# Optimization experiments

Hardware: AMD Instinct MI355X
Metric: run time of the kernel (lower is better)

Reference implementation:

```python
import jax, jax.numpy as jnp
import numpy as np

MODES = 32
WIDTH = 64
FACTOR = 2
N_LAYERS = 4


def dct_matrix(N):
    # Ortho DCT-II matrix D: dct(x) along last axis = x @ D.T ; idct(y) = y @ D
    n = jnp.arange(N, dtype=jnp.float32)
    k = n[:, None]
    D = jnp.cos(jnp.pi * (n[None, :] + 0.5) * k / N) * jnp.sqrt(2.0 / N)
    D = D.at[0].mul(1.0 / jnp.sqrt(2.0))
    return D


def setup_inputs() -> dict:
    key = jax.random.key(0)
    ks = jax.random.split(key, 16)
    B, M, N, IN_DIM = 4, 256, 256, 12
    hid = WIDTH * FACTOR
    xav_f = jnp.sqrt(2.0 / (WIDTH + WIDTH))  # xavier_normal for (in,out,modes)
    inp = {
        'x': jax.random.normal(ks[0], (B, M, N, IN_DIM), jnp.float32),
        'W_in': jax.random.normal(ks[1], (WIDTH, IN_DIM), jnp.float32) * (1.0 / jnp.sqrt(IN_DIM)),
        'b_in': jnp.zeros((WIDTH,), jnp.float32),
        'fw0': jax.random.normal(ks[2], (N_LAYERS, WIDTH, WIDTH, MODES), jnp.float32) * xav_f,
        'fw1': jax.random.normal(ks[3], (N_LAYERS, WIDTH, WIDTH, MODES), jnp.float32) * xav_f,
        'ffW1': jax.random.normal(ks[4], (N_LAYERS, hid, WIDTH), jnp.float32) * (1.0 / jnp.sqrt(WIDTH)),
        'ffb1': jnp.zeros((N_LAYERS, hid), jnp.float32),
        'ffW2': jax.random.normal(ks[5], (N_LAYERS, WIDTH, hid), jnp.float32) * (1.0 / jnp.sqrt(hid)),
        'ffb2': jnp.zeros((N_LAYERS, WIDTH), jnp.float32),
        'W_o1': jax.random.normal(ks[6], (128, WIDTH), jnp.float32) * (1.0 / jnp.sqrt(WIDTH)),
        'b_o1': jnp.zeros((128,), jnp.float32),
        'W_o2': jax.random.normal(ks[7], (1, 128), jnp.float32) * (1.0 / jnp.sqrt(128.0)),
        'b_o2': jnp.zeros((1,), jnp.float32),
    }
    return inp


def forward_fourier(x, w0, w1, DM, DN):
    # x: [B, M, N, I] channels-last -> [B, I, M, N]
    x = jnp.transpose(x, (0, 3, 1, 2))
    # --- y direction: DCT along N, truncated mode mix, IDCT ---
    x_fty = jnp.einsum('bimn,kn->bimk', x, DN)            # dct, [B,I,M,N]
    xy_m = jnp.einsum('bixy,ioy->boxy', x_fty[..., :MODES], w0)  # [B,O,M,modes]
    xy = jnp.einsum('boxy,yn->boxn', xy_m, DN[:MODES, :])        # idct of zero-padded spectrum
    # --- x direction: DCT along M ---
    x2 = jnp.swapaxes(x, -1, -2)                          # [B,I,N,M]
    x_ftx = jnp.einsum('binm,km->bink', x2, DM)
    xx_m = jnp.einsum('bixy,ioy->boxy', x_ftx[..., :MODES], w1)  # [B,O,N,modes]
    xx = jnp.einsum('boxy,ym->boxm', xx_m, DM[:MODES, :])        # [B,O,N,M]
    xx = jnp.swapaxes(xx, -1, -2)                         # [B,O,M,N]
    out = xx + xy
    return jnp.transpose(out, (0, 2, 3, 1))               # [B,M,N,O]


def feed_forward(h, W1, b1, W2, b2):
    h = jax.nn.relu(h @ W1.T + b1)
    return h @ W2.T + b2


def reference(x, W_in, b_in, fw0, fw1, ffW1, ffb1, ffW2, ffb2, W_o1, b_o1, W_o2, b_o2):
    B, M, N, _ = x.shape
    DM = dct_matrix(M)
    DN = dct_matrix(N)
    x = x @ W_in.T + b_in                                  # in_proj, [B,M,N,width]
    b = x
    for i in range(N_LAYERS):
        h = forward_fourier(x, fw0[i], fw1[i], DM, DN)
        b = feed_forward(h, ffW1[i], ffb1[i], ffW2[i], ffb2[i])
        x = x + b
    # use_fork=False: out applied to the LAST backcast b
    o = jax.nn.relu(b @ W_o1.T + b_o1) * 0 + (b @ W_o1.T + b_o1)  # WNLinear has no activation
    o = b @ W_o1.T + b_o1
    forecast = o @ W_o2.T + b_o2                           # [B,M,N,1]
    return forecast
```

## Files before the change

### kernel.cpp

```cpp
#include <hip/hip_runtime.h>
#include <hip/hip_bf16.h>
#include <math.h>

#define BATCH 4
#define MMDIM 256
#define NNDIM 256
#define CH 64
#define NMODES 32
#define HID 128
#define NLAYERS 4
#define XPLANE 16777216L

typedef __attribute__((ext_vector_type(8))) short bfrag;
typedef __attribute__((ext_vector_type(8))) ushort u16x8;
typedef __attribute__((ext_vector_type(4))) float f32x4;

__device__ inline ushort f2bf(float x) {
    union { float f; uint u; } v; v.f = x;
    uint r = v.u + 0x7fff + ((v.u >> 16) & 1);
    return (ushort)(r >> 16);
}
__device__ inline float bf2f(ushort h) {
    union { uint u; float f; } v; v.u = (uint)h << 16; return v.f;
}
__device__ inline void split(float v, ushort& hi, ushort& lo) {
    __hip_bfloat16 h = __float2bfloat16(v);
    hi = __builtin_bit_cast(ushort, h);
    lo = __builtin_bit_cast(ushort, __float2bfloat16(v - __bfloat162float(h)));
}
__device__ inline ushort f2bf_hw(float v) {
    return __builtin_bit_cast(ushort, __float2bfloat16(v));
}
#define MFMA __builtin_amdgcn_mfma_f32_16x16x32_bf16


__global__ __launch_bounds__(256) void k_Tfrag(ushort* __restrict__ Tf) {
    int idx = blockIdx.x * 256 + threadIdx.x;
    int j = idx & 7, lane = (idx >> 3) & 63, ks = (idx >> 9) & 7, yt = idx >> 12;
    int k = yt * 16 + (lane & 15);
    int n = ks * 32 + ((lane >> 4) << 3) + j;
    double v = cos(M_PI * (n + 0.5) * (double)k / 256.0) * 0.08838834764831845;
    if (k == 0) v *= 0.7071067811865476;
    float vf = (float)v;
    ushort hh = f2bf(vf);
    Tf[idx] = hh; Tf[idx + 8192] = f2bf(vf - bf2f(hh));
}

__global__ __launch_bounds__(256) void k_Ttfrag(ushort* __restrict__ Ttf) {
    int idx = blockIdx.x * 256 + threadIdx.x;
    int j = idx & 7, lane = (idx >> 3) & 63, at = idx >> 9;
    int k = ((lane >> 4) << 3) + j;
    int n = at * 16 + (lane & 15);
    double v = cos(M_PI * (n + 0.5) * (double)k / 256.0) * 0.08838834764831845;
    if (k == 0) v *= 0.7071067811865476;
    float vf = (float)v;
    ushort hh = f2bf(vf);
    Ttf[idx] = hh; Ttf[idx + 8192] = f2bf(vf - bf2f(hh));
}

__global__ __launch_bounds__(256) void k_wt(const float* __restrict__ fw0, const float* __restrict__ fw1,
                                            float* __restrict__ wt01) {
    int idx = blockIdx.x * 256 + threadIdx.x;
    const float* fw = (idx < 524288) ? fw0 : fw1;
    int i2 = idx & 524287;
    int l = i2 >> 17, r = i2 & 131071;
    int y = r >> 12, i = (r >> 6) & 63, o = r & 63;
    wt01[idx] = fw[((l * 64 + i) * 64 + o) * 32 + y];
}

__global__ __launch_bounds__(256) void k_wfrag(const float* __restrict__ W,
                                               ushort* __restrict__ hi, ushort* __restrict__ lo,
                                               int N, int K) {
    int idx = blockIdx.x * 256 + threadIdx.x;
    int per_l = N * K;
    int l = idx / per_l, r = idx % per_l;
    int jj = r & 7, lane = (r >> 3) & 63;
    int ks = (r >> 9) % (K >> 5);
    int nt = r / (512 * (K >> 5));
    int row = nt * 16 + (lane & 15);
    int col = ks * 32 + ((lane >> 4) << 3) + jj;
    float v = W[(long)l * per_l + row * K + col];
    ushort h = f2bf(v);
    hi[idx] = h;
    lo[idx] = f2bf(v - bf2f(h));
}

__global__ void k_head(const float* __restrict__ W_o1, const float* __restrict__ b_o1,
                       const float* __restrict__ W_o2, const float* __restrict__ b_o2,
                       float* __restrict__ Weff, float* __restrict__ beff) {
    int c = threadIdx.x;
    float acc = 0.f;
    for (int j = 0; j < 128; j++) acc += W_o2[j] * W_o1[j * 64 + c];
    Weff[c] = acc;
    if (c == 0) {
        float bb = 0.f;
        for (int j = 0; j < 128; j++) bb += W_o2[j] * b_o1[j];
        beff[0] = bb + b_o2[0];
    }
}

__global__ __launch_bounds__(256) void k_inproj_bf(const float* __restrict__ xin,
                                                   const float* __restrict__ W_in,
                                                   const float* __restrict__ b_in,
                                                   ushort* __restrict__ xbf) {
    __shared__ __align__(16) ushort tile[2][64][72];
    int t = threadIdx.x;
    int bid = blockIdx.x;
    int b = bid >> 10, m = (bid >> 2) & 255, n0 = (bid & 3) * 64;
    int c = t & 63, ng = t >> 6;
    long pbase = (long)(b * 256 + m) * 256 + n0;
    float w[12];
#pragma unroll
    for (int d = 0; d < 12; d++) w[d] = W_in[c * 12 + d];
    float bc = b_in[c];
#pragma unroll 4
    for (int i = 0; i < 16; i++) {
        int nl = ng * 16 + i;
        const float* xr = xin + (pbase + nl) * 12;
        float acc = bc;
#pragma unroll
        for (int d = 0; d < 12; d++) acc += xr[d] * w[d];
        ushort hh, ll;
        split(acc, hh, ll);
        tile[0][c][nl] = hh;
        tile[1][c][nl] = ll;
    }
    __syncthreads();
    int c2 = t >> 2, ch = t & 3;
#pragma unroll
    for (int pl = 0; pl < 2; pl++) {
        const ushort* s = &tile[pl][c2][ch * 16];
        u16x8 v0 = *(const u16x8*)s;
        u16x8 v1 = *(const u16x8*)(s + 8);
        ushort* dst = xbf + (long)pl * XPLANE + ((long)(b * 256 + m) * 64 + c2) * 256 + n0 + ch * 16;
        *(u16x8*)dst = v0; *(u16x8*)(dst + 8) = v1;
    }
}

__global__ __launch_bounds__(256) void k_tx(const ushort* __restrict__ src, ushort* __restrict__ dst) {
    __shared__ __align__(16) ushort tl[64][72];
    int t = threadIdx.x;
    int bid = blockIdx.x;
    int ntile = bid & 3, mt = (bid >> 2) & 3, c = (bid >> 4) & 63, b = (bid >> 10) & 3, pl = bid >> 12;
    int m0 = mt * 64, n0 = ntile * 64;
    const ushort* sp = src + (long)pl * XPLANE;
    ushort* dp = dst + (long)pl * XPLANE;
    {
        int row = t >> 2, ch = (t & 3) * 16;
        const ushort* p = sp + ((long)(b * 256 + m0 + row) * 64 + c) * 256 + n0 + ch;
        u16x8 v0 = *(const u16x8*)p;
        u16x8 v1 = *(const u16x8*)(p + 8);
#pragma unroll
        for (int k = 0; k < 8; k++) tl[ch + k][row] = v0[k];
#pragma unroll
        for (int k = 0; k < 8; k++) tl[ch + 8 + k][row] = v1[k];
    }
    __syncthreads();
    {
        int nrow = t >> 2, mch = (t & 3) * 16;
        const ushort* s = &tl[nrow][mch];
        u16x8 v0 = *(const u16x8*)s;
        u16x8 v1 = *(const u16x8*)(s + 8);
        ushort* p = dp + ((long)(b * 256 + n0 + nrow) * 64 + c) * 256 + m0 + mch;
        *(u16x8*)p = v0; *(u16x8*)(p + 8) = v1;
    }
}

__global__ __launch_bounds__(512) void k_spec(const ushort* __restrict__ xbf_y,
                                              const ushort* __restrict__ xbf_x,
                                              const ushort* __restrict__ Tf,
                                              const ushort* __restrict__ Ttf,
                                              const float* __restrict__ wt_y,
                                              const float* __restrict__ wt_x,
                                              float* __restrict__ hy,
                                              ushort* __restrict__ hx) {
    __shared__ float Xs[2][32][68];
    __shared__ __align__(16) ushort Xmb[2][2][64][40];
    int t = threadIdx.x;
    int lane = t & 63, wv = t >> 6, l15 = lane & 15, l4 = lane >> 4;
    int bid = blockIdx.x;
    int xpath = bid >> 9;
    int lb = bid & 511;
    int fp = lb & 127, b = lb >> 7;
    int s_ = wv >> 2;
    const ushort* xbf = xpath ? xbf_x : xbf_y;
    const float* wt = xpath ? wt_x : wt_y;

    {
        const ushort* xb = xbf + ((long)(b * 256 + fp * 2 + s_)) * 16384;
        f32x4 a0 = {0.f, 0.f, 0.f, 0.f}, a1 = {0.f, 0.f, 0.f, 0.f};
        int c0 = (wv & 3) * 16;
#pragma unroll
        for (int ks = 0; ks < 8; ks++) {
            const ushort* bp = xb + (c0 + l15) * 256 + ks * 32 + l4 * 8;
            bfrag bhi = *(const bfrag*)bp;
            bfrag blo = *(const bfrag*)(bp + XPLANE);
            const ushort* ap0 = Tf + (long)((0 * 8 + ks) * 64 + lane) * 8;
            const ushort* ap1 = Tf + (long)((1 * 8 + ks) * 64 + lane) * 8;
            bfrag a0h = *(const bfrag*)ap0, a0l = *(const bfrag*)(ap0 + 8192);
            bfrag a1h = *(const bfrag*)ap1, a1l = *(const bfrag*)(ap1 + 8192);
            a0 = MFMA(a0h, bhi, a0, 0, 0, 0);
            a0 = MFMA(a0h, blo, a0, 0, 0, 0);
            a0 = MFMA(a0l, bhi, a0, 0, 0, 0);
            a1 = MFMA(a1h, bhi, a1, 0, 0, 0);
            a1 = MFMA(a1h, blo, a1, 0, 0, 0);
            a1 = MFMA(a1l, bhi, a1, 0, 0, 0);
        }
#pragma unroll
        for (int r = 0; r < 4; r++) {
            Xs[s_][l4 * 4 + r][c0 + l15] = a0[r];
            Xs[s_][16 + l4 * 4 + r][c0 + l15] = a1[r];
        }
    }
    __syncthreads();

    {
        int og = t & 15, y = t >> 4;
        const float* wb = wt + (long)y * 4096 + og * 4;
        f32x4 A0 = {0.f, 0.f, 0.f, 0.f}, A1 = {0.f, 0.f, 0.f, 0.f};
#pragma unroll 8
        for (int i = 0; i < 64; i++) {
            float4 wv4 = *(const float4*)(wb + i * 64);
            float x0 = Xs[0][y][i];
            float x1 = Xs[1][y][i];
            A0.x += x0 * wv4.x; A0.y += x0 * wv4.y; A0.z += x0 * wv4.z; A0.w += x0 * wv4.w;
            A1.x += x1 * wv4.x; A1.y += x1 * wv4.y; A1.z += x1 * wv4.z; A1.w += x1 * wv4.w;
        }
#pragma unroll
        for (int e = 0; e < 4; e++) {
            ushort hh, ll;
            split(A0[e], hh, ll);
            Xmb[0][0][og * 4 + e][y] = hh;
            Xmb[0][1][og * 4 + e][y] = ll;
            split(A1[e], hh, ll);
            Xmb[1][0][og * 4 + e][y] = hh;
            Xmb[1][1][og * 4 + e][y] = ll;
        }
    }
    __syncthreads();

    bfrag vbh[4], vbl[4];
#pragma unroll
    for (int ot = 0; ot < 4; ot++) {
        vbh[ot] = *(const bfrag*)(&Xmb[s_][0][ot * 16 + l15][l4 * 8]);
        vbl[ot] = *(const bfrag*)(&Xmb[s_][1][ot * 16 + l15][l4 * 8]);
    }
    int f = fp * 2 + s_;
#pragma unroll
    for (int ai = 0; ai < 4; ai++) {
        int at = (wv & 3) * 4 + ai;
        const ushort* ap = Ttf + (long)(at * 64 + lane) * 8;
        bfrag th = *(const bfrag*)ap, tl_ = *(const bfrag*)(ap + 8192);
#pragma unroll
        for (int ot = 0; ot < 4; ot++) {
            f32x4 acc = {0.f, 0.f, 0.f, 0.f};
            acc = MFMA(th, vbh[ot], acc, 0, 0, 0);
            acc = MFMA(th, vbl[ot], acc, 0, 0, 0);
            acc = MFMA(tl_, vbh[ot], acc, 0, 0, 0);
            int arow = at * 16 + l4 * 4;
            if (!xpath) {
                float* op = hy + (long)b * 4194304 + (long)f * 16384 + (long)arow * 64 + ot * 16 + l15;
#pragma unroll
                for (int r = 0; r < 4; r++) op[r * 64] = acc[r];
            } else {
                ushort* op = hx + (long)b * 4194304 + (long)f * 64 + (long)arow * 16384 + ot * 16 + l15;
#pragma unroll
                for (int r = 0; r < 4; r++) op[(long)r * 16384] = f2bf_hw(acc[r]);
            }
        }
    }
}

#define ASW 136
__global__ __launch_bounds__(256) void k_ff(const float* __restrict__ hy,
                                            const ushort* __restrict__ hx,
                                            ushort* __restrict__ xbfw,
                                            const ushort* __restrict__ W1hi, const ushort* __restrict__ W1lo,
                                            const float* __restrict__ b1,
                                            const ushort* __restrict__ W2hi, const ushort* __restrict__ W2lo,
                                            const float* __restrict__ b2,
                                            const float* __restrict__ Weff, const float* __restrict__ beff,
                                            float* __restrict__ out, int last) {
    __shared__ __align__(16) ushort Asb[2][64][ASW];
    int t = threadIdx.x;
    int lane = t & 63, wv = t >> 6;
    int l15 = lane & 15, l4 = lane >> 4;
    long p0 = (long)blockIdx.x * 64;

    f32x4 acc1[8];
#pragma unroll
    for (int nt = 0; nt < 8; nt++) acc1[nt] = (f32x4){0.f, 0.f, 0.f, 0.f};
#pragma unroll
    for (int ks = 0; ks < 2; ks++) {
        long boff = (p0 + wv * 16 + l15) * 64 + ks * 32 + l4 * 8;
        const float* hp = hy + boff;
        float4 h0 = *(const float4*)hp;
        float4 h1 = *(const float4*)(hp + 4);
        u16x8 hx8 = *(const u16x8*)(hx + boff);
        bfrag ahi, alo;
#pragma unroll
        for (int j = 0; j < 8; j++) {
            float v = ((j < 4) ? (&h0.x)[j] : (&h1.x)[j - 4]) + bf2f(hx8[j]);
            ushort hh, ll;
            split(v, hh, ll);
            ahi[j] = (short)hh; alo[j] = (short)ll;
        }
#pragma unroll
        for (int nt = 0; nt < 8; nt++) {
            long off = (long)((nt * 2 + ks) * 64 + lane) * 8;
            bfrag bhi = *(const bfrag*)(W1hi + off);
            bfrag blo = *(const bfrag*)(W1lo + off);
            acc1[nt] = MFMA(ahi, bhi, acc1[nt], 0, 0, 0);
            acc1[nt] = MFMA(ahi, blo, acc1[nt], 0, 0, 0);
            acc1[nt] = MFMA(alo, bhi, acc1[nt], 0, 0, 0);
        }
    }
#pragma unroll
    for (int nt = 0; nt < 8; nt++) {
        float bj = b1[nt * 16 + l15];
        int j = nt * 16 + l15;
#pragma unroll
        for (int r = 0; r < 4; r++) {
            float v = fmaxf(acc1[nt][r] + bj, 0.f);
            int px = wv * 16 + l4 * 4 + r;
            ushort hh, ll;
            split(v, hh, ll);
            Asb[0][px][j] = hh;
            Asb[1][px][j] = ll;
        }
    }
    __syncthreads();

    f32x4 acc2[4];
#pragma unroll
    for (int nt = 0; nt < 4; nt++) acc2[nt] = (f32x4){0.f, 0.f, 0.f, 0.f};
#pragma unroll
    for (int ks = 0; ks < 4; ks++) {
        bfrag ahi = *(const bfrag*)(&Asb[0][wv * 16 + l15][ks * 32 + l4 * 8]);
        bfrag alo = *(const bfrag*)(&Asb[1][wv * 16 + l15][ks * 32 + l4 * 8]);
#pragma unroll
        for (int nt = 0; nt < 4; nt++) {
            long off = (long)((nt * 4 + ks) * 64 + lane) * 8;
            bfrag bhi = *(const bfrag*)(W2hi + off);
            bfrag blo = *(const bfrag*)(W2lo + off);
            acc2[nt] = MFMA(ahi, bhi, acc2[nt], 0, 0, 0);
            acc2[nt] = MFMA(ahi, blo, acc2[nt], 0, 0, 0);
            acc2[nt] = MFMA(alo, bhi, acc2[nt], 0, 0, 0);
        }
    }

    if (last) {
        float be = beff[0];
#pragma unroll
        for (int r = 0; r < 4; r++) {
            float v = 0.f;
#pragma unroll
            for (int nt = 0; nt < 4; nt++) {
                int c = nt * 16 + l15;
                v += (acc2[nt][r] + b2[c]) * Weff[c];
            }
            v += __shfl_xor(v, 1, 64);
            v += __shfl_xor(v, 2, 64);
            v += __shfl_xor(v, 4, 64);
            v += __shfl_xor(v, 8, 64);
            if (l15 == 0) out[p0 + wv * 16 + l4 * 4 + r] = v + be;
        }
    } else {
        __syncthreads();
        ushort* tile = &Asb[0][0][0];
        int b = (int)(p0 >> 16), m = (int)((p0 >> 8) & 255), n0 = (int)(p0 & 255);
        int c2 = t >> 2, ch = t & 3;
#pragma unroll
        for (int pl = 0; pl < 2; pl++) {
            const ushort* src = xbfw + (long)pl * XPLANE + ((long)(b * 256 + m) * 64 + c2) * 256 + n0 + ch * 16;
            u16x8 v0 = *(const u16x8*)src;
            u16x8 v1 = *(const u16x8*)(src + 8);
            ushort* d = tile + (pl * 64 + c2) * 72 + ch * 16;
            *(u16x8*)d = v0; *(u16x8*)(d + 8) = v1;
        }
        __syncthreads();
#pragma unroll
        for (int nt = 0; nt < 4; nt++) {
            int c = nt * 16 + l15;
            float bc = b2[c];
#pragma unroll
            for (int r = 0; r < 4; r++) {
                int nl = wv * 16 + l4 * 4 + r;
                float res = bf2f(tile[(0 * 64 + c) * 72 + nl]) + bf2f(tile[(1 * 64 + c) * 72 + nl]);
                float v = res + acc2[nt][r] + bc;
                ushort hh, ll;
                split(v, hh, ll);
                tile[(0 * 64 + c) * 72 + nl] = hh;
                tile[(1 * 64 + c) * 72 + nl] = ll;
            }
        }
        __syncthreads();
#pragma unroll
        for (int pl = 0; pl < 2; pl++) {
            const ushort* s = tile + (pl * 64 + c2) * 72 + ch * 16;
            u16x8 v0 = *(const u16x8*)s;
            u16x8 v1 = *(const u16x8*)(s + 8);
            ushort* dst = xbfw + (long)pl * XPLANE + ((long)(b * 256 + m) * 64 + c2) * 256 + n0 + ch * 16;
            *(u16x8*)dst = v0; *(u16x8*)(dst + 8) = v1;
        }
    }
}


extern "C" void kernel_launch(void* const* d_in, const int* in_sizes, int n_in,
                              void* d_out, int out_size, void* d_ws, size_t ws_size,
                              hipStream_t stream) {
    const float* x_in = (const float*)d_in[0];
    const float* W_in = (const float*)d_in[1];
    const float* b_in = (const float*)d_in[2];
    const float* fw0  = (const float*)d_in[3];
    const float* fw1  = (const float*)d_in[4];
    const float* ffW1 = (const float*)d_in[5];
    const float* ffb1 = (const float*)d_in[6];
    const float* ffW2 = (const float*)d_in[7];
    const float* ffb2 = (const float*)d_in[8];
    const float* W_o1 = (const float*)d_in[9];
    const float* b_o1 = (const float*)d_in[10];
    const float* W_o2 = (const float*)d_in[11];
    const float* b_o2 = (const float*)d_in[12];
    float* out = (float*)d_out;

    float* ws   = (float*)d_ws;
    float* w0t  = ws;
    float* w1t  = w0t + 524288;
    float* Weff = w1t + 524288;
    float* beff = Weff + 64;
    float* h_y  = beff + 64;
    ushort* h_x = (ushort*)(h_y + 16777216);
    ushort* Tfrag  = h_x + 16777216;
    ushort* Ttfrag = Tfrag + 16384;
    ushort* W1f_hi = Ttfrag + 16384;
    ushort* W1f_lo = W1f_hi + 32768;
    ushort* W2f_hi = W1f_lo + 32768;
    ushort* W2f_lo = W2f_hi + 32768;
    ushort* xbf_y  = W2f_lo + 32768;
    ushort* xbf_x  = xbf_y + 2 * XPLANE;

    k_Tfrag<<<32, 256, 0, stream>>>(Tfrag);
    k_Ttfrag<<<32, 256, 0, stream>>>(Ttfrag);
    k_wt<<<4096, 256, 0, stream>>>(fw0, fw1, w0t);
    k_wfrag<<<(NLAYERS * HID * CH) / 256, 256, 0, stream>>>(ffW1, W1f_hi, W1f_lo, HID, CH);
    k_wfrag<<<(NLAYERS * CH * HID) / 256, 256, 0, stream>>>(ffW2, W2f_hi, W2f_lo, CH, HID);
    k_head<<<1, 64, 0, stream>>>(W_o1, b_o1, W_o2, b_o2, Weff, beff);
    k_inproj_bf<<<4096, 256, 0, stream>>>(x_in, W_in, b_in, xbf_y);

    for (int l = 0; l < NLAYERS; l++) {
        k_tx<<<8192, 256, 0, stream>>>(xbf_y, xbf_x);
        k_spec<<<1024, 512, 0, stream>>>(xbf_y, xbf_x, Tfrag, Ttfrag,
                                         w0t + (long)l * 131072, w1t + (long)l * 131072,
                                         h_y, h_x);
        k_ff<<<4096, 256, 0, stream>>>(h_y, h_x, xbf_y,
            W1f_hi + (long)l * HID * CH, W1f_lo + (long)l * HID * CH,
            ffb1 + (long)l * HID,
            W2f_hi + (long)l * CH * HID, W2f_lo + (long)l * CH * HID,
            ffb2 + (long)l * CH,
            Weff, beff, out, (l == NLAYERS - 1) ? 1 : 0);
    }
}
```

Baseline: 664.4 us.

## Fuse transpose into feed-forward epilogue using 8x8 pixel tiles

The feed-forward kernel now processes 8x8 spatial tiles rather than 64-pixel row segments. This lets its epilogue write the updated residual both in y-major layout and transposed into the x-major buffer. The per-layer transpose kernel is removed, leaving one transpose after the input projection. The cost is shorter contiguous global accesses (16-byte runs instead of 64-byte runs) and more shared memory per block.

```diff
diff --git a/kernel.cpp b/kernel.cpp
--- a/kernel.cpp
+++ b/kernel.cpp
@@ -271,28 +271,32 @@
     }
 }
 
-#define ASW 136
 __global__ __launch_bounds__(256) void k_ff(const float* __restrict__ hy,
                                             const ushort* __restrict__ hx,
-                                            ushort* __restrict__ xbfw,
+                                            ushort* __restrict__ xbf_y,
+                                            ushort* __restrict__ xbf_x,
                                             const ushort* __restrict__ W1hi, const ushort* __restrict__ W1lo,
                                             const float* __restrict__ b1,
                                             const ushort* __restrict__ W2hi, const ushort* __restrict__ W2lo,
                                             const float* __restrict__ b2,
                                             const float* __restrict__ Weff, const float* __restrict__ beff,
                                             float* __restrict__ out, int last) {
-    __shared__ __align__(16) ushort Asb[2][64][ASW];
+    __shared__ __align__(16) ushort smem[18432];
     int t = threadIdx.x;
     int lane = t & 63, wv = t >> 6;
     int l15 = lane & 15, l4 = lane >> 4;
-    long p0 = (long)blockIdx.x * 64;
+    int bid = blockIdx.x;
+    int b = bid >> 10, mt = (bid >> 5) & 31, nt5 = bid & 31;
+    int m0 = mt * 8, n0 = nt5 * 8;
+    long pixbase = (long)b * 65536;
 
     f32x4 acc1[8];
 #pragma unroll
     for (int nt = 0; nt < 8; nt++) acc1[nt] = (f32x4){0.f, 0.f, 0.f, 0.f};
 #pragma unroll
     for (int ks = 0; ks < 2; ks++) {
-        long boff = (p0 + wv * 16 + l15) * 64 + ks * 32 + l4 * 8;
+        int px = wv * 16 + l15;
+        long boff = (pixbase + (long)(m0 + (px >> 3)) * 256 + n0 + (px & 7)) * 64 + ks * 32 + l4 * 8;
         const float* hp = hy + boff;
         float4 h0 = *(const float4*)hp;
         float4 h1 = *(const float4*)(hp + 4);
@@ -325,8 +329,8 @@
             int px = wv * 16 + l4 * 4 + r;
             ushort hh, ll;
             split(v, hh, ll);
-            Asb[0][px][j] = hh;
-            Asb[1][px][j] = ll;
+            smem[(0 * 64 + px) * 136 + j] = hh;
+            smem[(1 * 64 + px) * 136 + j] = ll;
         }
     }
     __syncthreads();
@@ -336,8 +340,9 @@
     for (int nt = 0; nt < 4; nt++) acc2[nt] = (f32x4){0.f, 0.f, 0.f, 0.f};
 #pragma unroll
     for (int ks = 0; ks < 4; ks++) {
-        bfrag ahi = *(const bfrag*)(&Asb[0][wv * 16 + l15][ks * 32 + l4 * 8]);
-        bfrag alo = *(const bfrag*)(&Asb[1][wv * 16 + l15][ks * 32 + l4 * 8]);
+        int px = wv * 16 + l15;
+        bfrag ahi = *(const bfrag*)(&smem[(0 * 64 + px) * 136 + ks * 32 + l4 * 8]);
+        bfrag alo = *(const bfrag*)(&smem[(1 * 64 + px) * 136 + ks * 32 + l4 * 8]);
 #pragma unroll
         for (int nt = 0; nt < 4; nt++) {
             long off = (long)((nt * 4 + ks) * 64 + lane) * 8;
@@ -363,20 +368,22 @@
             v += __shfl_xor(v, 2, 64);
             v += __shfl_xor(v, 4, 64);
             v += __shfl_xor(v, 8, 64);
-            if (l15 == 0) out[p0 + wv * 16 + l4 * 4 + r] = v + be;
+            if (l15 == 0) {
+                int px = wv * 16 + l4 * 4 + r;
+                out[pixbase + (long)(m0 + (px >> 3)) * 256 + n0 + (px & 7)] = v + be;
+            }
         }
     } else {
         __syncthreads();
-        ushort* tile = &Asb[0][0][0];
-        int b = (int)(p0 >> 16), m = (int)((p0 >> 8) & 255), n0 = (int)(p0 & 255);
-        int c2 = t >> 2, ch = t & 3;
-#pragma unroll
-        for (int pl = 0; pl < 2; pl++) {
-            const ushort* src = xbfw + (long)pl * XPLANE + ((long)(b * 256 + m) * 64 + c2) * 256 + n0 + ch * 16;
-            u16x8 v0 = *(const u16x8*)src;
-            u16x8 v1 = *(const u16x8*)(src + 8);
-            ushort* d = tile + (pl * 64 + c2) * 72 + ch * 16;
-            *(u16x8*)d = v0; *(u16x8*)(d + 8) = v1;
+        ushort* tileY = smem;
+        ushort* tileX = smem + 9216;
+#pragma unroll
+        for (int i = 0; i < 4; i++) {
+            int k = t + i * 256;
+            int pl = k >> 9, mloc = (k >> 6) & 7, c = k & 63;
+            const ushort* src = xbf_y + (long)pl * XPLANE
+                              + ((long)(b * 256 + m0 + mloc) * 64 + c) * 256 + n0;
+            *(u16x8*)&tileY[(pl * 64 + c) * 72 + mloc * 8] = *(const u16x8*)src;
         }
         __syncthreads();
 #pragma unroll
@@ -385,23 +392,29 @@
             float bc = b2[c];
 #pragma unroll
             for (int r = 0; r < 4; r++) {
-                int nl = wv * 16 + l4 * 4 + r;
-                float res = bf2f(tile[(0 * 64 + c) * 72 + nl]) + bf2f(tile[(1 * 64 + c) * 72 + nl]);
+                int px = wv * 16 + l4 * 4 + r;
+                float res = bf2f(tileY[(0 * 64 + c) * 72 + px]) + bf2f(tileY[(1 * 64 + c) * 72 + px]);
                 float v = res + acc2[nt][r] + bc;
                 ushort hh, ll;
                 split(v, hh, ll);
-                tile[(0 * 64 + c) * 72 + nl] = hh;
-                tile[(1 * 64 + c) * 72 + nl] = ll;
+                tileY[(0 * 64 + c) * 72 + px] = hh;
+                tileY[(1 * 64 + c) * 72 + px] = ll;
+                int xidx = (px & 7) * 8 + (px >> 3);
+                tileX[(0 * 64 + c) * 72 + xidx] = hh;
+                tileX[(1 * 64 + c) * 72 + xidx] = ll;
             }
         }
         __syncthreads();
 #pragma unroll
-        for (int pl = 0; pl < 2; pl++) {
-            const ushort* s = tile + (pl * 64 + c2) * 72 + ch * 16;
-            u16x8 v0 = *(const u16x8*)s;
-            u16x8 v1 = *(const u16x8*)(s + 8);
-            ushort* dst = xbfw + (long)pl * XPLANE + ((long)(b * 256 + m) * 64 + c2) * 256 + n0 + ch * 16;
-            *(u16x8*)dst = v0; *(u16x8*)(dst + 8) = v1;
+        for (int i = 0; i < 4; i++) {
+            int k = t + i * 256;
+            int pl = k >> 9, run = (k >> 6) & 7, c = k & 63;
+            ushort* dy = xbf_y + (long)pl * XPLANE
+                       + ((long)(b * 256 + m0 + run) * 64 + c) * 256 + n0;
+            *(u16x8*)dy = *(const u16x8*)&tileY[(pl * 64 + c) * 72 + run * 8];
+            ushort* dx = xbf_x + (long)pl * XPLANE
+                       + ((long)(b * 256 + n0 + run) * 64 + c) * 256 + m0;
+            *(u16x8*)dx = *(const u16x8*)&tileX[(pl * 64 + c) * 72 + run * 8];
         }
     }
 }
@@ -448,13 +461,13 @@
     k_wfrag<<<(NLAYERS * CH * HID) / 256, 256, 0, stream>>>(ffW2, W2f_hi, W2f_lo, CH, HID);
     k_head<<<1, 64, 0, stream>>>(W_o1, b_o1, W_o2, b_o2, Weff, beff);
     k_inproj_bf<<<4096, 256, 0, stream>>>(x_in, W_in, b_in, xbf_y);
+    k_tx<<<8192, 256, 0, stream>>>(xbf_y, xbf_x);
 
     for (int l = 0; l < NLAYERS; l++) {
-        k_tx<<<8192, 256, 0, stream>>>(xbf_y, xbf_x);
         k_spec<<<1024, 512, 0, stream>>>(xbf_y, xbf_x, Tfrag, Ttfrag,
                                          w0t + (long)l * 131072, w1t + (long)l * 131072,
                                          h_y, h_x);
-        k_ff<<<4096, 256, 0, stream>>>(h_y, h_x, xbf_y,
+        k_ff<<<4096, 256, 0, stream>>>(h_y, h_x, xbf_y, xbf_x,
             W1f_hi + (long)l * HID * CH, W1f_lo + (long)l * HID * CH,
             ffb1 + (long)l * HID,
             W2f_hi + (long)l * CH * HID, W2f_lo + (long)l * CH * HID,
```

After: 926.1 us. 39.4% more time.
